# Kernel optimization log

Hardware: AMD Instinct MI355X
Metric: run time of the kernel (lower is better)

Reference implementation:

```python
import jax, jax.numpy as jnp
import numpy as np

B, S, D = 1, 2048, 2048
H, KV, HD = 16, 4, 128
HALF = HD // 2
REP = H // KV
LAMBDA_INIT = 0.5
OUT_SCALE = 1.0 - LAMBDA_INIT


def _rope(x, cos, sin):
    # x: (B, S, heads, HD); cos/sin: (S, HD//2). Complex pair rotation on
    # interleaved (even, odd) channels, matching torch.view_as_complex.
    orig_shape = x.shape
    xp = x.reshape(*x.shape[:-1], -1, 2)
    x0, x1 = xp[..., 0], xp[..., 1]
    c = cos[None, :, None, :]
    s = sin[None, :, None, :]
    r0 = x0 * c - x1 * s
    r1 = x0 * s + x1 * c
    return jnp.stack([r0, r1], axis=-1).reshape(orig_shape)


def _sdpa_causal(q, k, v, scale):
    # q,k: (B, S, H, half), v: (B, S, H, HD). Causal softmax attention.
    scores = jnp.einsum('bshd,bthd->bhst', q, k) * scale
    causal = jnp.tril(jnp.ones((S, S), dtype=bool))
    scores = jnp.where(causal[None, None, :, :], scores, jnp.finfo(scores.dtype).min)
    p = jax.nn.softmax(scores, axis=-1)
    return jnp.einsum('bhst,bthd->bshd', p, v)


def setup_inputs() -> dict:
    key = jax.random.key(0)
    ks = jax.random.split(key, 7)
    x = jax.random.normal(ks[0], (B, S, D), dtype=jnp.float32)
    # RoPE frequencies: theta_i = 10000^(-2i/HD), angles = pos * theta
    inv_freq = 1.0 / (10000.0 ** (np.arange(0, HD, 2, dtype=np.float32) / HD))
    angles = np.arange(S, dtype=np.float32)[:, None] * inv_freq[None, :]
    freqs_cos = jnp.asarray(np.cos(angles), dtype=jnp.float32)
    freqs_sin = jnp.asarray(np.sin(angles), dtype=jnp.float32)
    sd = 0.02
    Wq = jax.random.normal(ks[1], (D, H * HD), dtype=jnp.float32) * sd
    Wk = jax.random.normal(ks[2], (D, KV * HD), dtype=jnp.float32) * sd
    Wv = jax.random.normal(ks[3], (D, KV * HD), dtype=jnp.float32) * sd
    Wo = jax.random.normal(ks[4], (H * HD, D), dtype=jnp.float32) * sd
    lam0 = float(np.log(LAMBDA_INIT / (1.0 - LAMBDA_INIT)))
    lambda_param = jnp.full((H,), lam0, dtype=jnp.float32)
    return {'x': x, 'freqs_cos': freqs_cos, 'freqs_sin': freqs_sin,
            'Wq': Wq, 'Wk': Wk, 'Wv': Wv, 'Wo': Wo, 'lambda_param': lambda_param}


def reference(x, freqs_cos, freqs_sin, Wq, Wk, Wv, Wo, lambda_param):
    q = (x @ Wq).reshape(B, S, H, HD)
    k = (x @ Wk).reshape(B, S, KV, HD)
    v = (x @ Wv).reshape(B, S, KV, HD)
    q = _rope(q, freqs_cos, freqs_sin)
    k = _rope(k, freqs_cos, freqs_sin)
    # GQA expansion: each kv head repeated REP times consecutively
    k = jnp.repeat(k, REP, axis=2)
    v = jnp.repeat(v, REP, axis=2)
    q1, q2 = q[..., :HALF], q[..., HALF:]
    k1, k2 = k[..., :HALF], k[..., HALF:]
    scale = 1.0 / jnp.sqrt(jnp.float32(HALF))  # SDPA scales by query last dim
    a1 = _sdpa_causal(q1, k1, v, scale)  # (B, S, H, HD)
    a2 = _sdpa_causal(q2, k2, v, scale)
    lam = jax.nn.sigmoid(lambda_param).astype(x.dtype)[None, None, :, None]
    out = (a1 - lam * a2) * OUT_SCALE
    out = out.reshape(B, S, H * HD)
    return out @ Wo
```

## Files before the change

kernel.cpp:

```cpp
#include <hip/hip_runtime.h>
#include <hip/hip_bf16.h>
#include <cstdint>

typedef __bf16 bf16_t;
typedef __attribute__((ext_vector_type(8))) __bf16 bf16x8;
typedef __attribute__((ext_vector_type(4))) __bf16 bf16x4;
typedef __attribute__((ext_vector_type(4))) float f32x4;

#define S_LEN 2048
#define D_MODEL 2048
#define NH 16
#define NKV 4
#define HD_ 128

#define MFMA16(a, b, c) __builtin_amdgcn_mfma_f32_16x16x32_bf16((a), (b), (c), 0, 0, 0)

__device__ __forceinline__ void gload_lds16(const void* g, void* l) {
  __builtin_amdgcn_global_load_lds((__attribute__((address_space(1))) void*)((void*)g),
                                   (__attribute__((address_space(3))) void*)(l), 16, 0, 0);
}

__global__ __launch_bounds__(256) void cast_x_kernel(const float* __restrict__ in,
                                                     bf16_t* __restrict__ out, int n8) {
  int i = blockIdx.x * 256 + threadIdx.x;
  if (i >= n8) return;
  float4 a = reinterpret_cast<const float4*>(in)[2 * i];
  float4 b = reinterpret_cast<const float4*>(in)[2 * i + 1];
  bf16x8 o = {(__bf16)a.x, (__bf16)a.y, (__bf16)a.z, (__bf16)a.w,
              (__bf16)b.x, (__bf16)b.y, (__bf16)b.z, (__bf16)b.w};
  *reinterpret_cast<bf16x8*>(out + (size_t)i * 8) = o;
}

__global__ __launch_bounds__(256) void transpose_cast64_kernel(const float* __restrict__ in,
    bf16_t* __restrict__ out, int ldin, int ldout) {
  __shared__ float t[64][65];
  const int c0 = blockIdx.x * 64, r0 = blockIdx.y * 64;
  const int rr = threadIdx.x >> 4;
  const int cc = (threadIdx.x & 15) * 4;
#pragma unroll
  for (int p = 0; p < 4; ++p) {
    int r = rr + p * 16;
    float4 v = *reinterpret_cast<const float4*>(in + (size_t)(r0 + r) * ldin + c0 + cc);
    t[r][cc] = v.x; t[r][cc + 1] = v.y; t[r][cc + 2] = v.z; t[r][cc + 3] = v.w;
  }
  __syncthreads();
  const int c = threadIdx.x >> 2;
  const int q = threadIdx.x & 3;
  bf16_t* orow = out + (size_t)(c0 + c) * ldout + r0 + q * 16;
#pragma unroll
  for (int half = 0; half < 2; ++half) {
    bf16x8 o;
#pragma unroll
    for (int j = 0; j < 8; ++j) o[j] = (__bf16)t[q * 16 + half * 8 + j][c];
    *reinterpret_cast<bf16x8*>(orow + half * 8) = o;
  }
}

#define SC_Q 0.18033688f

__global__ __launch_bounds__(256) void rope_kernel(const float* __restrict__ qkv,
    const float* __restrict__ cosT, const float* __restrict__ sinT,
    bf16_t* __restrict__ Qb, bf16_t* __restrict__ Kb) {
  const int s = blockIdx.x;
  const int tid = threadIdx.x;
  const int ch = tid & 15;
  float4 cs = *reinterpret_cast<const float4*>(cosT + s * 64 + ch * 4);
  float4 sn = *reinterpret_cast<const float4*>(sinT + s * 64 + ch * 4);
  {
    const int hq = tid >> 4;
    const float* src = qkv + (size_t)s * 3072 + hq * 128 + ch * 8;
    float4 a = *reinterpret_cast<const float4*>(src);
    float4 b = *reinterpret_cast<const float4*>(src + 4);
    bf16x8 o;
    o[0] = (__bf16)((a.x * cs.x - a.y * sn.x) * SC_Q);
    o[1] = (__bf16)((a.x * sn.x + a.y * cs.x) * SC_Q);
    o[2] = (__bf16)((a.z * cs.y - a.w * sn.y) * SC_Q);
    o[3] = (__bf16)((a.z * sn.y + a.w * cs.y) * SC_Q);
    o[4] = (__bf16)((b.x * cs.z - b.y * sn.z) * SC_Q);
    o[5] = (__bf16)((b.x * sn.z + b.y * cs.z) * SC_Q);
    o[6] = (__bf16)((b.z * cs.w - b.w * sn.w) * SC_Q);
    o[7] = (__bf16)((b.z * sn.w + b.w * cs.w) * SC_Q);
    *reinterpret_cast<bf16x8*>(Qb + ((size_t)hq * S_LEN + s) * HD_ + ch * 8) = o;
  }
  if (tid < 64) {
    const int kh = tid >> 4;
    const float* src = qkv + (size_t)s * 3072 + 2048 + kh * 128 + ch * 8;
    float4 a = *reinterpret_cast<const float4*>(src);
    float4 b = *reinterpret_cast<const float4*>(src + 4);
    bf16x8 o;
    o[0] = (__bf16)(a.x * cs.x - a.y * sn.x);
    o[1] = (__bf16)(a.x * sn.x + a.y * cs.x);
    o[2] = (__bf16)(a.z * cs.y - a.w * sn.y);
    o[3] = (__bf16)(a.z * sn.y + a.w * cs.y);
    o[4] = (__bf16)(b.x * cs.z - b.y * sn.z);
    o[5] = (__bf16)(b.x * sn.z + b.y * cs.z);
    o[6] = (__bf16)(b.z * cs.w - b.w * sn.w);
    o[7] = (__bf16)(b.z * sn.w + b.w * cs.w);
    *reinterpret_cast<bf16x8*>(Kb + ((size_t)kh * S_LEN + s) * HD_ + ch * 8) = o;
  }
}

#define BM 128
#define BN 128
#define BK 64

__global__ __launch_bounds__(256) void gemm_bf16_kernel(const bf16_t* __restrict__ A,
    const bf16_t* __restrict__ B, float* __restrict__ C, int M, int N, int K) {
  __shared__ __attribute__((aligned(16))) bf16_t aL[BM * BK];
  __shared__ __attribute__((aligned(16))) bf16_t bL[BN * BK];
  const int tid = threadIdx.x;
  const int wave = tid >> 6, lane = tid & 63;
  const int wr = wave >> 1, wc = wave & 1;
  const int l15 = lane & 15, l4 = lane >> 4;
  const int bm = blockIdx.y * BM, bn = blockIdx.x * BN;

  f32x4 zero = {0.f, 0.f, 0.f, 0.f};
  f32x4 acc[4][4];
#pragma unroll
  for (int m = 0; m < 4; ++m)
#pragma unroll
    for (int n = 0; n < 4; ++n) acc[m][n] = zero;

  const bf16_t* aSrc[4];
  const bf16_t* bSrc[4];
  bf16_t* aDst[4];
  bf16_t* bDst[4];
#pragma unroll
  for (int i = 0; i < 4; ++i) {
    int ci = i * 256 + tid;
    int r = ci >> 3;
    int cl = (ci & 7) ^ (r & 7);
    aSrc[i] = A + (size_t)(bm + r) * K + cl * 8;
    bSrc[i] = B + (size_t)(bn + r) * K + cl * 8;
    aDst[i] = aL + (i * 256 + wave * 64) * 8;
    bDst[i] = bL + (i * 256 + wave * 64) * 8;
  }

  for (int kt = 0; kt < K; kt += BK) {
#pragma unroll
    for (int i = 0; i < 4; ++i) gload_lds16(aSrc[i] + kt, aDst[i]);
#pragma unroll
    for (int i = 0; i < 4; ++i) gload_lds16(bSrc[i] + kt, bDst[i]);
    __syncthreads();
#pragma unroll
    for (int t = 0; t < 2; ++t) {
      bf16x8 af[4], bfr[4];
#pragma unroll
      for (int f = 0; f < 4; ++f) {
        int Ra = wr * 64 + f * 16 + l15;
        int ca = (t * 4 + l4) ^ (Ra & 7);
        af[f] = *reinterpret_cast<const bf16x8*>(aL + Ra * 64 + ca * 8);
        int Rb = wc * 64 + f * 16 + l15;
        int cb = (t * 4 + l4) ^ (Rb & 7);
        bfr[f] = *reinterpret_cast<const bf16x8*>(bL + Rb * 64 + cb * 8);
      }
#pragma unroll
      for (int m = 0; m < 4; ++m)
#pragma unroll
        for (int n = 0; n < 4; ++n) acc[m][n] = MFMA16(af[m], bfr[n], acc[m][n]);
    }
    __syncthreads();
  }

#pragma unroll
  for (int m = 0; m < 4; ++m) {
    int row0 = bm + wr * 64 + m * 16 + l4 * 4;
#pragma unroll
    for (int n = 0; n < 4; ++n) {
      int col = bn + wc * 64 + n * 16 + l15;
#pragma unroll
      for (int r = 0; r < 4; ++r) C[(size_t)(row0 + r) * N + col] = acc[m][n][r];
    }
  }
}

__global__ __launch_bounds__(256) void diff_attn_kernel(const bf16_t* __restrict__ Qb,
    const bf16_t* __restrict__ Kb, const bf16_t* __restrict__ VTb,
    const float* __restrict__ lambda_param, bf16_t* __restrict__ attn) {
  const int h = blockIdx.x;
  const int kvh = h >> 2;
  const int jt = (blockIdx.y < 16) ? (31 - blockIdx.y) : (blockIdx.y - 16);
  const int tid = threadIdx.x, wave = tid >> 6, lane = tid & 63;
  const int l15 = lane & 15, l4 = lane >> 4;

  __shared__ __attribute__((aligned(16))) bf16_t kB[2][64 * 128];
  __shared__ __attribute__((aligned(16))) bf16_t vB[2][64 * 128];
  __shared__ __attribute__((aligned(16))) bf16_t pS[4][2][16 * 64];

  const bf16_t* kBase = Kb + (size_t)kvh * S_LEN * HD_;
  const bf16_t* vBase = VTb + (size_t)kvh * HD_ * S_LEN;
  int kOff[4], vOff[4], dOff[4];
#pragma unroll
  for (int i = 0; i < 4; ++i) {
    int ci = i * 256 + tid;
    int kr = ci >> 4;
    kOff[i] = kr * HD_ + (((ci & 15) ^ (kr & 7)) * 8);
    int vr = ci >> 3;
    vOff[i] = vr * S_LEN + (((ci & 7) ^ (vr & 7)) * 8);
    dOff[i] = (i * 256 + wave * 64) * 8;
  }

  const float lam = 1.f / (1.f + __expf(-lambda_param[h]));
  const f32x4 zero = {0.f, 0.f, 0.f, 0.f};

  const int q0 = jt * 64;
  const int qg = q0 + wave * 16 + l15;

  const bf16_t* qp = Qb + ((size_t)h * S_LEN + qg) * HD_;
  bf16x8 qf[4];
#pragma unroll
  for (int f = 0; f < 4; ++f) qf[f] = *reinterpret_cast<const bf16x8*>(qp + f * 32 + l4 * 8);

  f32x4 o1[8], o2[8];
#pragma unroll
  for (int n = 0; n < 8; ++n) { o1[n] = zero; o2[n] = zero; }
  float m1 = -__builtin_inff(), m2 = -__builtin_inff(), l1 = 0.f, l2 = 0.f;

#pragma unroll
  for (int i = 0; i < 4; ++i) gload_lds16(kBase + kOff[i], &kB[0][0] + dOff[i]);
#pragma unroll
  for (int i = 0; i < 4; ++i) gload_lds16(vBase + vOff[i], &vB[0][0] + dOff[i]);
  __syncthreads();

  for (int t = 0; t <= jt; ++t) {
    const int cur = t & 1;
    if (t < jt) {
      const size_t kv0n = (size_t)(t + 1) * 64;
#pragma unroll
      for (int i = 0; i < 4; ++i) gload_lds16(kBase + kv0n * HD_ + kOff[i], &kB[cur ^ 1][0] + dOff[i]);
#pragma unroll
      for (int i = 0; i < 4; ++i) gload_lds16(vBase + kv0n + vOff[i], &vB[cur ^ 1][0] + dOff[i]);
    }
    const bf16_t* kL = &kB[cur][0];
    const bf16_t* vL = &vB[cur][0];
    const int kv0 = t * 64;

    f32x4 s1[4], s2[4];
#pragma unroll
    for (int n = 0; n < 4; ++n) { s1[n] = zero; s2[n] = zero; }
#pragma unroll
    for (int tt = 0; tt < 2; ++tt) {
#pragma unroll
      for (int n = 0; n < 4; ++n) {
        const int Rk = n * 16 + l15;
        bf16x8 kf1 = *reinterpret_cast<const bf16x8*>(kL + Rk * 128 + (((tt * 4 + l4) ^ (Rk & 7)) * 8));
        s1[n] = MFMA16(kf1, qf[tt], s1[n]);
      }
    }
#pragma unroll
    for (int tt = 0; tt < 2; ++tt) {
#pragma unroll
      for (int n = 0; n < 4; ++n) {
        const int Rk = n * 16 + l15;
        bf16x8 kf2 = *reinterpret_cast<const bf16x8*>(kL + Rk * 128 + (((8 + tt * 4 + l4) ^ (Rk & 7)) * 8));
        s2[n] = MFMA16(kf2, qf[2 + tt], s2[n]);
      }
    }

    if (t == jt) {
#pragma unroll
      for (int n = 0; n < 4; ++n)
#pragma unroll
        for (int r = 0; r < 4; ++r)
          if (kv0 + n * 16 + l4 * 4 + r > qg) { s1[n][r] = -1e30f; s2[n][r] = -1e30f; }
    }

    {
      float tmax = s1[0][0];
#pragma unroll
      for (int n = 0; n < 4; ++n)
#pragma unroll
        for (int r = 0; r < 4; ++r) tmax = fmaxf(tmax, s1[n][r]);
      tmax = fmaxf(tmax, __shfl_xor(tmax, 16));
      tmax = fmaxf(tmax, __shfl_xor(tmax, 32));
      if (!__all(tmax <= m1 + 8.f)) {
        const float mn = fmaxf(m1, tmax);
        const float sc = __builtin_exp2f(m1 - mn);
        m1 = mn;
        l1 *= sc;
#pragma unroll
        for (int n = 0; n < 8; ++n) o1[n] *= sc;
      }
      float rs = 0.f;
#pragma unroll
      for (int n = 0; n < 4; ++n) {
        float e0 = __builtin_exp2f(s1[n][0] - m1);
        float e1 = __builtin_exp2f(s1[n][1] - m1);
        float e2 = __builtin_exp2f(s1[n][2] - m1);
        float e3 = __builtin_exp2f(s1[n][3] - m1);
        rs += (e0 + e1) + (e2 + e3);
        int cswz = (n * 2 + (l4 >> 1)) ^ (l15 & 7);
        bf16x4 pk = {(__bf16)e0, (__bf16)e1, (__bf16)e2, (__bf16)e3};
        *reinterpret_cast<bf16x4*>(&pS[wave][0][l15 * 64 + cswz * 8 + (l4 & 1) * 4]) = pk;
      }
      rs += __shfl_xor(rs, 16);
      rs += __shfl_xor(rs, 32);
      l1 += rs;
    }
    {
      float tmax = s2[0][0];
#pragma unroll
      for (int n = 0; n < 4; ++n)
#pragma unroll
        for (int r = 0; r < 4; ++r) tmax = fmaxf(tmax, s2[n][r]);
      tmax = fmaxf(tmax, __shfl_xor(tmax, 16));
      tmax = fmaxf(tmax, __shfl_xor(tmax, 32));
      if (!__all(tmax <= m2 + 8.f)) {
        const float mn = fmaxf(m2, tmax);
        const float sc = __builtin_exp2f(m2 - mn);
        m2 = mn;
        l2 *= sc;
#pragma unroll
        for (int n = 0; n < 8; ++n) o2[n] *= sc;
      }
      float rs = 0.f;
#pragma unroll
      for (int n = 0; n < 4; ++n) {
        float e0 = __builtin_exp2f(s2[n][0] - m2);
        float e1 = __builtin_exp2f(s2[n][1] - m2);
        float e2 = __builtin_exp2f(s2[n][2] - m2);
        float e3 = __builtin_exp2f(s2[n][3] - m2);
        rs += (e0 + e1) + (e2 + e3);
        int cswz = (n * 2 + (l4 >> 1)) ^ (l15 & 7);
        bf16x4 pk = {(__bf16)e0, (__bf16)e1, (__bf16)e2, (__bf16)e3};
        *reinterpret_cast<bf16x4*>(&pS[wave][1][l15 * 64 + cswz * 8 + (l4 & 1) * 4]) = pk;
      }
      rs += __shfl_xor(rs, 16);
      rs += __shfl_xor(rs, 32);
      l2 += rs;
    }

#pragma unroll
    for (int kt = 0; kt < 2; ++kt) {
      int cp = ((kt * 4 + l4) ^ (l15 & 7)) * 8;
      bf16x8 pf1 = *reinterpret_cast<const bf16x8*>(&pS[wave][0][l15 * 64 + cp]);
      bf16x8 pf2 = *reinterpret_cast<const bf16x8*>(&pS[wave][1][l15 * 64 + cp]);
#pragma unroll
      for (int n = 0; n < 8; ++n) {
        const int Rv = n * 16 + l15;
        bf16x8 vf = *reinterpret_cast<const bf16x8*>(vL + Rv * 64 + (((kt * 4 + l4) ^ (Rv & 7)) * 8));
        o1[n] = MFMA16(vf, pf1, o1[n]);
        o2[n] = MFMA16(vf, pf2, o2[n]);
      }
    }
    __syncthreads();
  }

  const float i1 = 1.f / l1, i2 = lam / l2;
  bf16_t* orow = attn + (size_t)qg * D_MODEL + h * HD_;
#pragma unroll
  for (int n = 0; n < 8; ++n) {
    bf16x4 w = {(__bf16)((o1[n][0] * i1 - o2[n][0] * i2) * 0.5f),
                (__bf16)((o1[n][1] * i1 - o2[n][1] * i2) * 0.5f),
                (__bf16)((o1[n][2] * i1 - o2[n][2] * i2) * 0.5f),
                (__bf16)((o1[n][3] * i1 - o2[n][3] * i2) * 0.5f)};
    *reinterpret_cast<bf16x4*>(orow + n * 16 + l4 * 4) = w;
  }
}

extern "C" void kernel_launch(void* const* d_in, const int* in_sizes, int n_in,
                              void* d_out, int out_size, void* d_ws, size_t ws_size,
                              hipStream_t stream) {
  const float* x    = (const float*)d_in[0];
  const float* fcos = (const float*)d_in[1];
  const float* fsin = (const float*)d_in[2];
  const float* Wq   = (const float*)d_in[3];
  const float* Wk   = (const float*)d_in[4];
  const float* Wv   = (const float*)d_in[5];
  const float* Wo   = (const float*)d_in[6];
  const float* lam  = (const float*)d_in[7];
  float* out = (float*)d_out;

  char* w = (char*)d_ws;
  bf16_t* xb    = (bf16_t*)(w);
  bf16_t* attnb = (bf16_t*)(w);
  bf16_t* WqkvT = (bf16_t*)(w + (8ull << 20));
  bf16_t* Qb    = (bf16_t*)(w + (8ull << 20));
  bf16_t* Kb    = (bf16_t*)(w + (16ull << 20));
  bf16_t* VT    = (bf16_t*)(w + (18ull << 20));
  bf16_t* WoT   = (bf16_t*)(w + (20ull << 20));
  float*  QKV   = (float*) (w + (28ull << 20));

  cast_x_kernel<<<2048, 256, 0, stream>>>(x, xb, 524288);
  transpose_cast64_kernel<<<dim3(32, 32), 256, 0, stream>>>(Wq, WqkvT, 2048, 2048);
  transpose_cast64_kernel<<<dim3(8, 32), 256, 0, stream>>>(Wk, WqkvT + 2048 * 2048, 512, 2048);
  transpose_cast64_kernel<<<dim3(8, 32), 256, 0, stream>>>(Wv, WqkvT + 2560 * 2048, 512, 2048);
  transpose_cast64_kernel<<<dim3(32, 32), 256, 0, stream>>>(Wo, WoT, 2048, 2048);

  gemm_bf16_kernel<<<dim3(24, 16), 256, 0, stream>>>(xb, WqkvT, QKV, 2048, 3072, 2048);

  rope_kernel<<<2048, 256, 0, stream>>>(QKV, fcos, fsin, Qb, Kb);
  transpose_cast64_kernel<<<dim3(8, 32), 256, 0, stream>>>(QKV + 2560, VT, 3072, 2048);

  diff_attn_kernel<<<dim3(16, 32), 256, 0, stream>>>(Qb, Kb, VT, lam, attnb);

  gemm_bf16_kernel<<<dim3(16, 16), 256, 0, stream>>>(attnb, WoT, out, 2048, 2048, 2048);
}
```

Baseline: 306.9 us.

## Use narrower GEMM tiles, reorder attention grid, add MFMA priority hints

The GEMM becomes a template on N-tile width, and both projection GEMMs use 128x64 tiles, which doubles the block count on the device's many compute units. The attention grid is flattened so long and short causal tiles alternate in launch order for better load balance. s_setprio hints are wrapped around the MFMA sections, and the softmax max/sum reductions become tree-shaped to shorten dependency chains. Narrower tiles lower arithmetic intensity per block and mean more A-tile reloads.

```diff
diff --git a/kernel.cpp b/kernel.cpp
--- a/kernel.cpp
+++ b/kernel.cpp
@@ -101,38 +101,46 @@
 }
 
 #define BM 128
-#define BN 128
 #define BK 64
 
+template <int BNv>
 __global__ __launch_bounds__(256) void gemm_bf16_kernel(const bf16_t* __restrict__ A,
     const bf16_t* __restrict__ B, float* __restrict__ C, int M, int N, int K) {
+  constexpr int NF = BNv / 32;
+  constexpr int BITER = BNv * 8 / 256;
   __shared__ __attribute__((aligned(16))) bf16_t aL[BM * BK];
-  __shared__ __attribute__((aligned(16))) bf16_t bL[BN * BK];
+  __shared__ __attribute__((aligned(16))) bf16_t bL[BNv * BK];
   const int tid = threadIdx.x;
   const int wave = tid >> 6, lane = tid & 63;
   const int wr = wave >> 1, wc = wave & 1;
   const int l15 = lane & 15, l4 = lane >> 4;
-  const int bm = blockIdx.y * BM, bn = blockIdx.x * BN;
+  const int bm = blockIdx.y * BM, bn = blockIdx.x * BNv;
 
   f32x4 zero = {0.f, 0.f, 0.f, 0.f};
-  f32x4 acc[4][4];
+  f32x4 acc[4][NF];
 #pragma unroll
   for (int m = 0; m < 4; ++m)
 #pragma unroll
-    for (int n = 0; n < 4; ++n) acc[m][n] = zero;
+    for (int n = 0; n < NF; ++n) acc[m][n] = zero;
 
   const bf16_t* aSrc[4];
-  const bf16_t* bSrc[4];
   bf16_t* aDst[4];
-  bf16_t* bDst[4];
 #pragma unroll
   for (int i = 0; i < 4; ++i) {
     int ci = i * 256 + tid;
     int r = ci >> 3;
     int cl = (ci & 7) ^ (r & 7);
     aSrc[i] = A + (size_t)(bm + r) * K + cl * 8;
+    aDst[i] = aL + (i * 256 + wave * 64) * 8;
+  }
+  const bf16_t* bSrc[BITER];
+  bf16_t* bDst[BITER];
+#pragma unroll
+  for (int i = 0; i < BITER; ++i) {
+    int ci = i * 256 + tid;
+    int r = ci >> 3;
+    int cl = (ci & 7) ^ (r & 7);
     bSrc[i] = B + (size_t)(bn + r) * K + cl * 8;
-    aDst[i] = aL + (i * 256 + wave * 64) * 8;
     bDst[i] = bL + (i * 256 + wave * 64) * 8;
   }
 
@@ -140,24 +148,29 @@
 #pragma unroll
     for (int i = 0; i < 4; ++i) gload_lds16(aSrc[i] + kt, aDst[i]);
 #pragma unroll
-    for (int i = 0; i < 4; ++i) gload_lds16(bSrc[i] + kt, bDst[i]);
+    for (int i = 0; i < BITER; ++i) gload_lds16(bSrc[i] + kt, bDst[i]);
     __syncthreads();
 #pragma unroll
     for (int t = 0; t < 2; ++t) {
-      bf16x8 af[4], bfr[4];
+      bf16x8 af[4], bfr[NF];
 #pragma unroll
       for (int f = 0; f < 4; ++f) {
         int Ra = wr * 64 + f * 16 + l15;
         int ca = (t * 4 + l4) ^ (Ra & 7);
         af[f] = *reinterpret_cast<const bf16x8*>(aL + Ra * 64 + ca * 8);
-        int Rb = wc * 64 + f * 16 + l15;
+      }
+#pragma unroll
+      for (int f = 0; f < NF; ++f) {
+        int Rb = wc * (BNv / 2) + f * 16 + l15;
         int cb = (t * 4 + l4) ^ (Rb & 7);
         bfr[f] = *reinterpret_cast<const bf16x8*>(bL + Rb * 64 + cb * 8);
       }
+      __builtin_amdgcn_s_setprio(1);
 #pragma unroll
       for (int m = 0; m < 4; ++m)
 #pragma unroll
-        for (int n = 0; n < 4; ++n) acc[m][n] = MFMA16(af[m], bfr[n], acc[m][n]);
+        for (int n = 0; n < NF; ++n) acc[m][n] = MFMA16(af[m], bfr[n], acc[m][n]);
+      __builtin_amdgcn_s_setprio(0);
     }
     __syncthreads();
   }
@@ -166,8 +179,8 @@
   for (int m = 0; m < 4; ++m) {
     int row0 = bm + wr * 64 + m * 16 + l4 * 4;
 #pragma unroll
-    for (int n = 0; n < 4; ++n) {
-      int col = bn + wc * 64 + n * 16 + l15;
+    for (int n = 0; n < NF; ++n) {
+      int col = bn + wc * (BNv / 2) + n * 16 + l15;
 #pragma unroll
       for (int r = 0; r < 4; ++r) C[(size_t)(row0 + r) * N + col] = acc[m][n][r];
     }
@@ -177,9 +190,12 @@
 __global__ __launch_bounds__(256) void diff_attn_kernel(const bf16_t* __restrict__ Qb,
     const bf16_t* __restrict__ Kb, const bf16_t* __restrict__ VTb,
     const float* __restrict__ lambda_param, bf16_t* __restrict__ attn) {
-  const int h = blockIdx.x;
+  const int b = blockIdx.x;
+  const int p = b >> 1;
+  const int h = p >> 4;
+  const int tdx = p & 15;
+  const int jt = (b & 1) ? tdx : (31 - tdx);
   const int kvh = h >> 2;
-  const int jt = (blockIdx.y < 16) ? (31 - blockIdx.y) : (blockIdx.y - 16);
   const int tid = threadIdx.x, wave = tid >> 6, lane = tid & 63;
   const int l15 = lane & 15, l4 = lane >> 4;
 
@@ -238,6 +254,7 @@
     f32x4 s1[4], s2[4];
 #pragma unroll
     for (int n = 0; n < 4; ++n) { s1[n] = zero; s2[n] = zero; }
+    __builtin_amdgcn_s_setprio(1);
 #pragma unroll
     for (int tt = 0; tt < 2; ++tt) {
 #pragma unroll
@@ -256,6 +273,7 @@
         s2[n] = MFMA16(kf2, qf[2 + tt], s2[n]);
       }
     }
+    __builtin_amdgcn_s_setprio(0);
 
     if (t == jt) {
 #pragma unroll
@@ -266,11 +284,11 @@
     }
 
     {
-      float tmax = s1[0][0];
+      float ma[4];
 #pragma unroll
       for (int n = 0; n < 4; ++n)
-#pragma unroll
-        for (int r = 0; r < 4; ++r) tmax = fmaxf(tmax, s1[n][r]);
+        ma[n] = fmaxf(fmaxf(s1[n][0], s1[n][1]), fmaxf(s1[n][2], s1[n][3]));
+      float tmax = fmaxf(fmaxf(ma[0], ma[1]), fmaxf(ma[2], ma[3]));
       tmax = fmaxf(tmax, __shfl_xor(tmax, 16));
       tmax = fmaxf(tmax, __shfl_xor(tmax, 32));
       if (!__all(tmax <= m1 + 8.f)) {
@@ -281,28 +299,29 @@
 #pragma unroll
         for (int n = 0; n < 8; ++n) o1[n] *= sc;
       }
-      float rs = 0.f;
+      float rsn[4];
 #pragma unroll
       for (int n = 0; n < 4; ++n) {
         float e0 = __builtin_exp2f(s1[n][0] - m1);
         float e1 = __builtin_exp2f(s1[n][1] - m1);
         float e2 = __builtin_exp2f(s1[n][2] - m1);
         float e3 = __builtin_exp2f(s1[n][3] - m1);
-        rs += (e0 + e1) + (e2 + e3);
+        rsn[n] = (e0 + e1) + (e2 + e3);
         int cswz = (n * 2 + (l4 >> 1)) ^ (l15 & 7);
         bf16x4 pk = {(__bf16)e0, (__bf16)e1, (__bf16)e2, (__bf16)e3};
         *reinterpret_cast<bf16x4*>(&pS[wave][0][l15 * 64 + cswz * 8 + (l4 & 1) * 4]) = pk;
       }
+      float rs = (rsn[0] + rsn[1]) + (rsn[2] + rsn[3]);
       rs += __shfl_xor(rs, 16);
       rs += __shfl_xor(rs, 32);
       l1 += rs;
     }
     {
-      float tmax = s2[0][0];
+      float ma[4];
 #pragma unroll
       for (int n = 0; n < 4; ++n)
-#pragma unroll
-        for (int r = 0; r < 4; ++r) tmax = fmaxf(tmax, s2[n][r]);
+        ma[n] = fmaxf(fmaxf(s2[n][0], s2[n][1]), fmaxf(s2[n][2], s2[n][3]));
+      float tmax = fmaxf(fmaxf(ma[0], ma[1]), fmaxf(ma[2], ma[3]));
       tmax = fmaxf(tmax, __shfl_xor(tmax, 16));
       tmax = fmaxf(tmax, __shfl_xor(tmax, 32));
       if (!__all(tmax <= m2 + 8.f)) {
@@ -313,23 +332,25 @@
 #pragma unroll
         for (int n = 0; n < 8; ++n) o2[n] *= sc;
       }
-      float rs = 0.f;
+      float rsn[4];
 #pragma unroll
       for (int n = 0; n < 4; ++n) {
         float e0 = __builtin_exp2f(s2[n][0] - m2);
         float e1 = __builtin_exp2f(s2[n][1] - m2);
         float e2 = __builtin_exp2f(s2[n][2] - m2);
         float e3 = __builtin_exp2f(s2[n][3] - m2);
-        rs += (e0 + e1) + (e2 + e3);
+        rsn[n] = (e0 + e1) + (e2 + e3);
         int cswz = (n * 2 + (l4 >> 1)) ^ (l15 & 7);
         bf16x4 pk = {(__bf16)e0, (__bf16)e1, (__bf16)e2, (__bf16)e3};
         *reinterpret_cast<bf16x4*>(&pS[wave][1][l15 * 64 + cswz * 8 + (l4 & 1) * 4]) = pk;
       }
+      float rs = (rsn[0] + rsn[1]) + (rsn[2] + rsn[3]);
       rs += __shfl_xor(rs, 16);
       rs += __shfl_xor(rs, 32);
       l2 += rs;
     }
 
+    __builtin_amdgcn_s_setprio(1);
 #pragma unroll
     for (int kt = 0; kt < 2; ++kt) {
       int cp = ((kt * 4 + l4) ^ (l15 & 7)) * 8;
@@ -343,6 +364,7 @@
         o2[n] = MFMA16(vf, pf2, o2[n]);
       }
     }
+    __builtin_amdgcn_s_setprio(0);
     __syncthreads();
   }
 
@@ -387,12 +409,12 @@
   transpose_cast64_kernel<<<dim3(8, 32), 256, 0, stream>>>(Wv, WqkvT + 2560 * 2048, 512, 2048);
   transpose_cast64_kernel<<<dim3(32, 32), 256, 0, stream>>>(Wo, WoT, 2048, 2048);
 
-  gemm_bf16_kernel<<<dim3(24, 16), 256, 0, stream>>>(xb, WqkvT, QKV, 2048, 3072, 2048);
+  gemm_bf16_kernel<64><<<dim3(48, 16), 256, 0, stream>>>(xb, WqkvT, QKV, 2048, 3072, 2048);
 
   rope_kernel<<<2048, 256, 0, stream>>>(QKV, fcos, fsin, Qb, Kb);
   transpose_cast64_kernel<<<dim3(8, 32), 256, 0, stream>>>(QKV + 2560, VT, 3072, 2048);
 
-  diff_attn_kernel<<<dim3(16, 32), 256, 0, stream>>>(Qb, Kb, VT, lam, attnb);
-
-  gemm_bf16_kernel<<<dim3(16, 16), 256, 0, stream>>>(attnb, WoT, out, 2048, 2048, 2048);
-}
+  diff_attn_kernel<<<512, 256, 0, stream>>>(Qb, Kb, VT, lam, attnb);
+
+  gemm_bf16_kernel<64><<<dim3(32, 16), 256, 0, stream>>>(attnb, WoT, out, 2048, 2048, 2048);
+}
```

Measured after the change: 286.5 us. -6.7%, faster.
